# Optimization experiments

Measured on AMD Instinct MI355X. Metric: run time of the kernel, lower is better.

## Reference

```python
import jax, jax.numpy as jnp
import numpy as np

N = 4096
NFEAT = 1024
NHID = 512
NCLS = 32
NLAYERS = 3
SPARSITY = 0.002


def _l2norm(x, eps=1e-12):
    n = jnp.sqrt(jnp.sum(x * x, axis=1, keepdims=True))
    return x / jnp.maximum(n, eps)


def setup_inputs() -> dict:
    key = jax.random.key(0)
    ks = jax.random.split(key, 12)
    # sparse-valued dense adjacency (original stores torch.sparse but densifies every hop)
    vals = jax.random.uniform(ks[0], (N, N), dtype=jnp.float32)
    mask = jax.random.uniform(ks[1], (N, N)) < SPARSITY
    adj = jnp.where(mask, vals, 0.0)
    features = jax.random.normal(ks[2], (N, NFEAT), dtype=jnp.float32)
    # y is a one-hot label matrix [N, nclass]
    labels = jax.random.randint(ks[3], (N,), 0, NCLS)
    y = jax.nn.one_hot(labels, NCLS, dtype=jnp.float32)
    s = 0.02
    W0 = jax.random.normal(ks[4], (NFEAT + 3 * NCLS, NHID), dtype=jnp.float32) * s
    b0 = jnp.zeros((NHID,), jnp.float32)
    W1_0 = jax.random.normal(ks[5], (NHID + 3 * NCLS, NHID), dtype=jnp.float32) * s
    b1_0 = jnp.zeros((NHID,), jnp.float32)
    W1_1 = jax.random.normal(ks[6], (NHID + 3 * NCLS, NHID), dtype=jnp.float32) * s
    b1_1 = jnp.zeros((NHID,), jnp.float32)
    W2 = jax.random.normal(ks[7], (NFEAT + NHID, NCLS), dtype=jnp.float32) * s
    b2 = jnp.zeros((NCLS,), jnp.float32)
    alphas = jnp.ones((NLAYERS, 5), jnp.float32)
    return {
        "adj": adj, "features": features, "y": y,
        "W0": W0, "b0": b0, "W1_0": W1_0, "b1_0": b1_0,
        "W1_1": W1_1, "b1_1": b1_1, "W2": W2, "b2": b2,
        "alphas": alphas, "layer_norm": 1,
    }


def reference(adj, features, y, W0, b0, W1_0, b1_0, W1_1, b1_1, W2, b2, alphas, layer_norm):
    Ws = [(W0, b0), (W1_0, b1_0), (W1_1, b1_1)]
    initial_features = jax.lax.stop_gradient(features)  # .clone().detach()
    feats = features
    max_features = None
    pow_adj = adj  # persists across layers (faithful to original): hops adj, adj^2, adj^4
    for i in range(NLAYERS):
        mask_alpha = jax.nn.softmax(alphas[i], axis=0)
        for _ in range(i):
            pow_adj = adj @ pow_adj
        hop = pow_adj @ feats                                   # [N, d]
        dist = (pow_adj > 0).astype(adj.dtype)                  # binarized reachability
        y_out = dist @ y                                        # [N, c]
        y_in = dist.T @ y                                       # [N, c]
        y_all = y_in + y_out
        hop = mask_alpha[0] * hop
        y_out = mask_alpha[1] * y_out
        y_in = mask_alpha[2] * y_in
        y_all = mask_alpha[3] * y_all
        mat = jnp.concatenate([hop, y_out, y_in, y_all], axis=1)
        W, b = Ws[i]
        tmp = mat @ W + b
        if layer_norm:
            tmp = _l2norm(tmp)
        feats = tmp
        max_features = tmp if max_features is None else jnp.maximum(max_features, tmp)
    final_mat = jnp.concatenate([initial_features, max_features], axis=1)
    out = jax.nn.relu(final_mat)
    # dropout: eval mode (identity)
    out = out @ W2 + b2
    return jax.nn.log_softmax(out, axis=1)
```

## Files before the change

kernel.cpp:

```cpp
#include <hip/hip_runtime.h>
#include <hip/hip_bf16.h>
#include <math.h>

typedef unsigned long long u64;
typedef unsigned short ushort_t;
typedef float f32x4 __attribute__((ext_vector_type(4)));
typedef short s16x8 __attribute__((ext_vector_type(8)));

#define NN 4096
#define NF 1024
#define NH 512
#define NC 32
#define LDP 40
#define K0 (NF + 3*NC)
#define K1 (NH + 3*NC)

__device__ inline float bf2f(ushort_t u) {
    unsigned int v = ((unsigned int)u) << 16;
    return __uint_as_float(v);
}
__device__ inline ushort_t f2bf(float f) {
    __hip_bfloat16 h = __float2bfloat16(f);
    return *(ushort_t*)&h;
}

__global__ __launch_bounds__(64) void k_build(const float* __restrict__ adj, u64* __restrict__ B1,
                                              int* __restrict__ rowcnt, int* __restrict__ colidx,
                                              float* __restrict__ vals) {
    int i = blockIdx.x;
    int l = threadIdx.x;
    const float* row = adj + (size_t)i * NN + l * 64;
    const float4* row4 = (const float4*)row;
    u64 w = 0;
    #pragma unroll
    for (int k = 0; k < 16; ++k) {
        float4 v = row4[k];
        if (v.x > 0.f) w |= 1ULL << (4*k + 0);
        if (v.y > 0.f) w |= 1ULL << (4*k + 1);
        if (v.z > 0.f) w |= 1ULL << (4*k + 2);
        if (v.w > 0.f) w |= 1ULL << (4*k + 3);
    }
    B1[(size_t)i*64 + l] = w;
    int cnt = __popcll(w);
    int pre = cnt;
    #pragma unroll
    for (int o = 1; o < 64; o <<= 1) {
        int u = __shfl_up(pre, o, 64);
        if (l >= o) pre += u;
    }
    int excl = pre - cnt;
    int total = __shfl(pre, 63, 64);
    u64 ww = w;
    int idx = excl;
    while (ww) {
        int b = __ffsll((unsigned long long)ww) - 1;
        ww &= ww - 1;
        if (idx < 64) {
            colidx[i*64 + idx] = l*64 + b;
            vals[i*64 + idx] = row[b];
        }
        ++idx;
    }
    int tot = total < 64 ? total : 64;
    for (int s = tot + l; s < 64; s += 64) {
        colidx[i*64 + s] = 0;
        vals[i*64 + s] = 0.f;
    }
    if (l == 0) {
        int r4 = (tot + 3) & ~3;
        rowcnt[i] = r4 < 64 ? r4 : 64;
    }
}

__global__ __launch_bounds__(256) void k_prep(const float* __restrict__ features,
                                              __hip_bfloat16* __restrict__ featb,
                                              const float* __restrict__ y, u64* __restrict__ LC,
                                              const float* __restrict__ W0,
                                              const float* __restrict__ W1_0,
                                              const float* __restrict__ W1_1,
                                              __hip_bfloat16* __restrict__ Wt0,
                                              __hip_bfloat16* __restrict__ Wt1,
                                              __hip_bfloat16* __restrict__ Wt2,
                                              const float* __restrict__ alphas,
                                              float* __restrict__ a_sm) {
    __shared__ float tile[32][33];
    int b = blockIdx.x;
    int t = threadIdx.x;
    if (b < 4096) {
        int base = b * 1024 + t * 4;
        float4 v = *(const float4*)&features[base];
        ushort4 o;
        o.x = f2bf(v.x); o.y = f2bf(v.y); o.z = f2bf(v.z); o.w = f2bf(v.w);
        *(ushort4*)&((ushort_t*)featb)[base] = o;
    } else if (b < 4112) {
        int w = (b - 4096) * 4 + (t >> 6);
        int l = t & 63;
        const float* yr = y + (size_t)(w*64 + l) * NC;
        for (int c = 0; c < NC; ++c) {
            u64 m = __ballot(yr[c] > 0.5f);
            if (l == c) LC[c*64 + w] = m;
        }
    } else {
        const float* W; __hip_bfloat16* Wt; int K, ktiles, idx;
        if (b < 4672)      { W = W0;   Wt = Wt0; K = K0; ktiles = 35; idx = b - 4112; }
        else if (b < 4976) { W = W1_0; Wt = Wt1; K = K1; ktiles = 19; idx = b - 4672; }
        else if (b < 5280) { W = W1_1; Wt = Wt2; K = K1; ktiles = 19; idx = b - 4976; }
        else {
            if (t == 0) {
                for (int i = 0; i < 3; ++i) {
                    float m = -1e30f;
                    for (int j = 0; j < 5; ++j) m = fmaxf(m, alphas[i*5+j]);
                    float e[5]; float s = 0.f;
                    for (int j = 0; j < 5; ++j) { e[j] = expf(alphas[i*5+j] - m); s += e[j]; }
                    for (int j = 0; j < 5; ++j) a_sm[i*5+j] = e[j] / s;
                }
            }
            return;
        }
        int kb = (idx % ktiles) * 32, nb = (idx / ktiles) * 32;
        int tc = t & 31, tr8 = t >> 5;
        for (int r = tr8; r < 32; r += 8)
            tile[r][tc] = W[(size_t)(kb + r) * NH + nb + tc];
        __syncthreads();
        ushort_t* Wu = (ushort_t*)Wt;
        for (int r = tr8; r < 32; r += 8)
            Wu[(size_t)(nb + r) * K + kb + tc] = f2bf(tile[tc][r]);
    }
}

__global__ __launch_bounds__(256) void k_bsquare(const u64* __restrict__ Bidx,
                                                 const u64* __restrict__ Bdat,
                                                 u64* __restrict__ Bout) {
    int i = blockIdx.x;
    int t = threadIdx.x;
    int wid = t >> 6, lane = t & 63;
    __shared__ u64 ridx[64];
    __shared__ u64 part[4][64];
    if (t < 64) ridx[t] = Bidx[(size_t)i*64 + t];
    __syncthreads();
    u64 acc = 0;
    for (int u = wid*16; u < wid*16 + 16; ++u) {
        u64 w = ridx[u];
        while (w) {
            int k = u*64 + (__ffsll((unsigned long long)w) - 1);
            w &= (w - 1);
            acc |= Bdat[(size_t)k*64 + lane];
        }
    }
    part[wid][lane] = acc;
    __syncthreads();
    if (t < 64) Bout[(size_t)i*64 + t] = part[0][t] | part[1][t] | part[2][t] | part[3][t];
}

__global__ void k_btrans(const u64* __restrict__ B1, const u64* __restrict__ B2,
                         const u64* __restrict__ B4, u64* __restrict__ B1T,
                         u64* __restrict__ B2T, u64* __restrict__ B4T) {
    const u64* B; u64* BT;
    switch (blockIdx.z) {
        case 0: B = B1; BT = B1T; break;
        case 1: B = B2; BT = B2T; break;
        default: B = B4; BT = B4T; break;
    }
    int I = blockIdx.x, J = blockIdx.y;
    int t = threadIdx.x;
    __shared__ u64 ld[64];
    ld[t] = B[(size_t)(I*64 + t)*64 + J];
    __syncthreads();
    u64 out = 0;
    for (int r = 0; r < 64; ++r) out |= ((ld[r] >> t) & 1ULL) << r;
    BT[(size_t)(J*64 + t)*64 + I] = out;
}

__global__ __launch_bounds__(256) void k_ymat(const u64* __restrict__ B1, const u64* __restrict__ B1T,
                       const u64* __restrict__ B2, const u64* __restrict__ B2T,
                       const u64* __restrict__ B4, const u64* __restrict__ B4T,
                       const u64* __restrict__ LC, const float* __restrict__ a_sm,
                       __hip_bfloat16* __restrict__ mat0, __hip_bfloat16* __restrict__ mat1,
                       __hip_bfloat16* __restrict__ mat2) {
    int layer = blockIdx.y;
    const u64 *B, *BT; const float* asp; ushort_t* m; int d, K;
    if (layer == 0)      { B = B1; BT = B1T; asp = a_sm;      m = (ushort_t*)mat0; d = NF; K = K0; }
    else if (layer == 1) { B = B2; BT = B2T; asp = a_sm + 5;  m = (ushort_t*)mat1; d = NH; K = K1; }
    else                 { B = B4; BT = B4T; asp = a_sm + 10; m = (ushort_t*)mat2; d = NH; K = K1; }
    __shared__ u64 LCt[64 * 32];
    __shared__ u64 rows[8][64], rowsT[8][64];
    int rb = blockIdx.x * 8;
    int t = threadIdx.x;
    for (int k = t; k < 2048; k += 256) {
        int c = k >> 6, w = k & 63;
        LCt[w*32 + c] = LC[k];
    }
    for (int k = t; k < 512; k += 256) {
        int r = k >> 6, w = k & 63;
        rows[r][w]  = B[(size_t)(rb + r)*64 + w];
        rowsT[r][w] = BT[(size_t)(rb + r)*64 + w];
    }
    __syncthreads();
    int wid = t >> 6, lane = t & 63;
    int h = lane >> 5, c = lane & 31;
    int r = wid * 2 + h;
    int co = 0, ci = 0;
    #pragma unroll
    for (int w = 0; w < 64; ++w) {
        u64 lc = LCt[w*32 + c];
        co += __popcll(rows[r][w]  & lc);
        ci += __popcll(rowsT[r][w] & lc);
    }
    float a1 = asp[1], a2 = asp[2], a3 = asp[3];
    size_t i = rb + r;
    m[i*K + d + c]      = f2bf(a1 * (float)co);
    m[i*K + d + 32 + c] = f2bf(a2 * (float)ci);
    m[i*K + d + 64 + c] = f2bf(a3 * (float)(co + ci));
}

__global__ void k_spmm(const int* __restrict__ rowcnt, const int* __restrict__ colidx,
                       const float* __restrict__ vals, const __hip_bfloat16* __restrict__ X,
                       __hip_bfloat16* __restrict__ Y, int d, int ystride,
                       const float* __restrict__ a_sm, int ai) {
    int i = blockIdx.x * 4 + threadIdx.y;
    int t = threadIdx.x;
    int cnt = rowcnt[i];
    const ushort_t* Xu = (const ushort_t*)X;
    float acc[8] = {0,0,0,0,0,0,0,0};
    for (int p = 0; p < cnt; p += 4) {
        int4   cc = *(const int4*)&colidx[i*64 + p];
        float4 vv = *(const float4*)&vals[i*64 + p];
        s16x8 x0 = *(const s16x8*)&Xu[(size_t)cc.x * d + 8*t];
        s16x8 x1 = *(const s16x8*)&Xu[(size_t)cc.y * d + 8*t];
        s16x8 x2 = *(const s16x8*)&Xu[(size_t)cc.z * d + 8*t];
        s16x8 x3 = *(const s16x8*)&Xu[(size_t)cc.w * d + 8*t];
        #pragma unroll
        for (int j = 0; j < 8; ++j) {
            acc[j] += vv.x * bf2f((ushort_t)x0[j]);
            acc[j] += vv.y * bf2f((ushort_t)x1[j]);
            acc[j] += vv.z * bf2f((ushort_t)x2[j]);
            acc[j] += vv.w * bf2f((ushort_t)x3[j]);
        }
    }
    float alpha = (ai >= 0) ? a_sm[ai] : 1.0f;
    s16x8 o;
    #pragma unroll
    for (int j = 0; j < 8; ++j) o[j] = (short)f2bf(alpha * acc[j]);
    *(s16x8*)&((ushort_t*)Y)[(size_t)i*ystride + 8*t] = o;
}

__global__ __launch_bounds__(256) void k_gemm_mfma(const __hip_bfloat16* __restrict__ mat,
                                                   const __hip_bfloat16* __restrict__ Wt,
                                                   const float* __restrict__ b,
                                                   float* __restrict__ C, int K) {
    __shared__ ushort_t As[64 * LDP];
    __shared__ ushort_t Bs[64 * LDP];
    int bx = blockIdx.x;
    int xcd = bx & 7, rest = bx >> 3;
    int nt = rest & 7, mt = (rest >> 3) * 8 + xcd;
    int bm = mt * 64, bn = nt * 64;
    int tid = threadIdx.x;
    int srow = tid >> 2, scol = (tid & 3) * 8;
    int wid = tid >> 6, lane = tid & 63;
    int fr = lane & 15, fk = (lane >> 4) * 8;
    f32x4 acc[4] = {{0,0,0,0},{0,0,0,0},{0,0,0,0},{0,0,0,0}};
    const ushort_t* Au = (const ushort_t*)mat + (size_t)(bm + srow) * K + scol;
    const ushort_t* Bu = (const ushort_t*)Wt  + (size_t)(bn + srow) * K + scol;
    for (int k0 = 0; k0 < K; k0 += 32) {
        *(s16x8*)&As[srow * LDP + scol] = *(const s16x8*)(Au + k0);
        *(s16x8*)&Bs[srow * LDP + scol] = *(const s16x8*)(Bu + k0);
        __syncthreads();
        s16x8 af = *(const s16x8*)&As[(wid * 16 + fr) * LDP + fk];
        #pragma unroll
        for (int j = 0; j < 4; ++j) {
            s16x8 bfv = *(const s16x8*)&Bs[(j * 16 + fr) * LDP + fk];
            acc[j] = __builtin_amdgcn_mfma_f32_16x16x32_bf16(af, bfv, acc[j], 0, 0, 0);
        }
        __syncthreads();
    }
    int drow = bm + wid * 16 + (lane >> 4) * 4;
    #pragma unroll
    for (int j = 0; j < 4; ++j) {
        int col = bn + j * 16 + fr;
        float bias = b[col];
        #pragma unroll
        for (int r = 0; r < 4; ++r)
            C[(size_t)(drow + r) * NH + col] = acc[j][r] + bias;
    }
}

__global__ void k_l2norm(const float* __restrict__ tmp, __hip_bfloat16* __restrict__ featsb,
                         float* __restrict__ maxf, const int* __restrict__ lnflag,
                         int first) {
    int i = blockIdx.x;
    int t = threadIdx.x;
    float v0 = tmp[(size_t)i*NH + t];
    float v1 = tmp[(size_t)i*NH + 256 + t];
    float ss = v0*v0 + v1*v1;
    __shared__ float red[4];
    #pragma unroll
    for (int o = 32; o > 0; o >>= 1) ss += __shfl_down(ss, o, 64);
    if ((t & 63) == 0) red[t >> 6] = ss;
    __syncthreads();
    float tot = red[0] + red[1] + red[2] + red[3];
    float scale = 1.0f;
    if (*lnflag) {
        float n = sqrtf(tot);
        scale = 1.0f / fmaxf(n, 1e-12f);
    }
    v0 *= scale; v1 *= scale;
    ushort_t* fb = (ushort_t*)featsb;
    fb[(size_t)i*NH + t]       = f2bf(v0);
    fb[(size_t)i*NH + 256 + t] = f2bf(v1);
    if (first) {
        maxf[(size_t)i*NH + t] = v0;
        maxf[(size_t)i*NH + 256 + t] = v1;
    } else {
        maxf[(size_t)i*NH + t] = fmaxf(maxf[(size_t)i*NH + t], v0);
        maxf[(size_t)i*NH + 256 + t] = fmaxf(maxf[(size_t)i*NH + 256 + t], v1);
    }
}

__global__ __launch_bounds__(256) void k_l2final(const float* __restrict__ tmpo,
                                                 const float* __restrict__ maxf,
                                                 const float* __restrict__ feat0,
                                                 const float* __restrict__ W2,
                                                 const float* __restrict__ b2,
                                                 const int* __restrict__ lnflag,
                                                 float* __restrict__ out) {
    int rb = blockIdx.x * 8;
    int t = threadIdx.x;
    __shared__ float rows[8][NF + NH];
    __shared__ float part[8][8][32];
    for (int r = 0; r < 8; ++r) {
        const float* f0 = feat0 + (size_t)(rb + r) * NF;
        for (int c = t; c < NF; c += 256) rows[r][c] = fmaxf(f0[c], 0.f);
    }
    int wid = t >> 6, lane = t & 63;
    int ln = *lnflag;
    #pragma unroll
    for (int rr = 0; rr < 2; ++rr) {
        int r = wid * 2 + rr;
        const float4* tp = (const float4*)(tmpo + (size_t)(rb + r) * NH + lane * 8);
        float4 va = tp[0], vb = tp[1];
        float ss = va.x*va.x + va.y*va.y + va.z*va.z + va.w*va.w
                 + vb.x*vb.x + vb.y*vb.y + vb.z*vb.z + vb.w*vb.w;
        #pragma unroll
        for (int o = 32; o > 0; o >>= 1) ss += __shfl_xor(ss, o, 64);
        float scale = ln ? 1.0f / fmaxf(sqrtf(ss), 1e-12f) : 1.0f;
        const float4* mf = (const float4*)(maxf + (size_t)(rb + r) * NH + lane * 8);
        float4 ma = mf[0], mb = mf[1];
        float* dst = &rows[r][NF + lane * 8];
        dst[0] = fmaxf(fmaxf(ma.x, va.x*scale), 0.f);
        dst[1] = fmaxf(fmaxf(ma.y, va.y*scale), 0.f);
        dst[2] = fmaxf(fmaxf(ma.z, va.z*scale), 0.f);
        dst[3] = fmaxf(fmaxf(ma.w, va.w*scale), 0.f);
        dst[4] = fmaxf(fmaxf(mb.x, vb.x*scale), 0.f);
        dst[5] = fmaxf(fmaxf(mb.y, vb.y*scale), 0.f);
        dst[6] = fmaxf(fmaxf(mb.z, vb.z*scale), 0.f);
        dst[7] = fmaxf(fmaxf(mb.w, vb.w*scale), 0.f);
    }
    __syncthreads();
    int c = t & 31, g = t >> 5;
    float acc[8] = {0,0,0,0,0,0,0,0};
    for (int k = g * 192; k < (g + 1) * 192; ++k) {
        float w = W2[(size_t)k * NC + c];
        #pragma unroll
        for (int r = 0; r < 8; ++r) acc[r] += rows[r][k] * w;
    }
    #pragma unroll
    for (int r = 0; r < 8; ++r) part[g][r][c] = acc[r];
    __syncthreads();
    int r = g;
    float lg = b2[c];
    #pragma unroll
    for (int gg = 0; gg < 8; ++gg) lg += part[gg][r][c];
    float m = lg;
    #pragma unroll
    for (int o = 16; o > 0; o >>= 1) m = fmaxf(m, __shfl_xor(m, o, 32));
    float e = expf(lg - m), s = e;
    #pragma unroll
    for (int o = 16; o > 0; o >>= 1) s += __shfl_xor(s, o, 32);
    out[(size_t)(rb + r) * NC + c] = lg - m - logf(s);
}

extern "C" void kernel_launch(void* const* d_in, const int* in_sizes, int n_in,
                              void* d_out, int out_size, void* d_ws, size_t ws_size,
                              hipStream_t stream) {
    const float* adj      = (const float*)d_in[0];
    const float* features = (const float*)d_in[1];
    const float* y        = (const float*)d_in[2];
    const float* W0       = (const float*)d_in[3];
    const float* b0       = (const float*)d_in[4];
    const float* W1_0     = (const float*)d_in[5];
    const float* b1_0     = (const float*)d_in[6];
    const float* W1_1     = (const float*)d_in[7];
    const float* b1_1     = (const float*)d_in[8];
    const float* W2       = (const float*)d_in[9];
    const float* b2       = (const float*)d_in[10];
    const float* alphas   = (const float*)d_in[11];
    const int*   lnflag   = (const int*)d_in[12];
    float* out = (float*)d_out;

    char* ws = (char*)d_ws;
    size_t off = 0;
    auto alloc = [&](size_t bytes) -> char* {
        char* p = ws + off;
        off = (off + bytes + 255) & ~(size_t)255;
        return p;
    };
    float* a_sm   = (float*)alloc(16 * 4);
    int*   rowcnt = (int*)alloc((size_t)NN * 4);
    int*   colidx = (int*)alloc((size_t)NN * 64 * 4);
    float* vals   = (float*)alloc((size_t)NN * 64 * 4);
    u64* B1  = (u64*)alloc((size_t)NN * 64 * 8);
    u64* B2  = (u64*)alloc((size_t)NN * 64 * 8);
    u64* B4  = (u64*)alloc((size_t)NN * 64 * 8);
    u64* B1T = (u64*)alloc((size_t)NN * 64 * 8);
    u64* B2T = (u64*)alloc((size_t)NN * 64 * 8);
    u64* B4T = (u64*)alloc((size_t)NN * 64 * 8);
    u64* LC  = (u64*)alloc((size_t)NC * 64 * 8);
    __hip_bfloat16* featb  = (__hip_bfloat16*)alloc((size_t)NN * NF * 2);
    __hip_bfloat16* featsb = (__hip_bfloat16*)alloc((size_t)NN * NH * 2);
    __hip_bfloat16* t1b    = (__hip_bfloat16*)alloc((size_t)NN * NH * 2);
    __hip_bfloat16* mat0   = (__hip_bfloat16*)alloc((size_t)NN * K0 * 2);
    __hip_bfloat16* mat1   = (__hip_bfloat16*)alloc((size_t)NN * K1 * 2);
    __hip_bfloat16* mat2   = (__hip_bfloat16*)alloc((size_t)NN * K1 * 2);
    __hip_bfloat16* Wt0    = (__hip_bfloat16*)alloc((size_t)NH * K0 * 2);
    __hip_bfloat16* Wt1    = (__hip_bfloat16*)alloc((size_t)NH * K1 * 2);
    __hip_bfloat16* Wt2    = (__hip_bfloat16*)alloc((size_t)NH * K1 * 2);
    float* tmpo = (float*)alloc((size_t)NN * NH * 4);
    float* maxf = (float*)alloc((size_t)NN * NH * 4);
    __hip_bfloat16* t2b = (__hip_bfloat16*)tmpo;

    k_build<<<NN, 64, 0, stream>>>(adj, B1, rowcnt, colidx, vals);
    k_prep<<<5281, 256, 0, stream>>>(features, featb, y, LC, W0, W1_0, W1_1,
                                     Wt0, Wt1, Wt2, alphas, a_sm);
    k_bsquare<<<NN, 256, 0, stream>>>(B1, B1, B2);
    k_bsquare<<<NN, 256, 0, stream>>>(B2, B2, B4);
    k_btrans<<<dim3(64, 64, 3), 64, 0, stream>>>(B1, B2, B4, B1T, B2T, B4T);
    k_ymat<<<dim3(NN/8, 3), 256, 0, stream>>>(B1, B1T, B2, B2T, B4, B4T, LC, a_sm,
                                              mat0, mat1, mat2);

    k_spmm<<<NN/4, dim3(NF/8, 4), 0, stream>>>(rowcnt, colidx, vals, featb, mat0, NF, K0, a_sm, 0);
    k_gemm_mfma<<<512, 256, 0, stream>>>(mat0, Wt0, b0, tmpo, K0);
    k_l2norm<<<NN, 256, 0, stream>>>(tmpo, featsb, maxf, lnflag, 1);

    k_spmm<<<NN/4, dim3(NH/8, 4), 0, stream>>>(rowcnt, colidx, vals, featsb, t1b, NH, NH, a_sm, -1);
    k_spmm<<<NN/4, dim3(NH/8, 4), 0, stream>>>(rowcnt, colidx, vals, t1b, mat1, NH, K1, a_sm, 5);
    k_gemm_mfma<<<512, 256, 0, stream>>>(mat1, Wt1, b1_0, tmpo, K1);
    k_l2norm<<<NN, 256, 0, stream>>>(tmpo, featsb, maxf, lnflag, 0);

    k_spmm<<<NN/4, dim3(NH/8, 4), 0, stream>>>(rowcnt, colidx, vals, featsb, t1b, NH, NH, a_sm, -1);
    k_spmm<<<NN/4, dim3(NH/8, 4), 0, stream>>>(rowcnt, colidx, vals, t1b, t2b, NH, NH, a_sm, -1);
    k_spmm<<<NN/4, dim3(NH/8, 4), 0, stream>>>(rowcnt, colidx, vals, t2b, t1b, NH, NH, a_sm, -1);
    k_spmm<<<NN/4, dim3(NH/8, 4), 0, stream>>>(rowcnt, colidx, vals, t1b, mat2, NH, K1, a_sm, 10);
    k_gemm_mfma<<<512, 256, 0, stream>>>(mat2, Wt2, b1_1, tmpo, K1);

    k_l2final<<<NN/8, 256, 0, stream>>>(tmpo, maxf, features, W2, b2, lnflag, out);
}
```

Baseline: 223.3 us.

## Fuse pipeline into multi-role phase kernels with precomputed A² sparse matrix

```diff
diff --git a/kernel.cpp b/kernel.cpp
--- a/kernel.cpp
+++ b/kernel.cpp
@@ -24,11 +24,10 @@
     return *(ushort_t*)&h;
 }
 
-__global__ __launch_bounds__(64) void k_build(const float* __restrict__ adj, u64* __restrict__ B1,
-                                              int* __restrict__ rowcnt, int* __restrict__ colidx,
-                                              float* __restrict__ vals) {
-    int i = blockIdx.x;
-    int l = threadIdx.x;
+__device__ void role_build(int i, int l, const float* __restrict__ adj,
+                           u64* __restrict__ B1, int* __restrict__ rowcnt,
+                           int* __restrict__ rowcnt_true,
+                           int* __restrict__ colidx, float* __restrict__ vals) {
     const float* row = adj + (size_t)i * NN + l * 64;
     const float4* row4 = (const float4*)row;
     u64 w = 0;
@@ -67,56 +66,46 @@
         vals[i*64 + s] = 0.f;
     }
     if (l == 0) {
-        int r4 = (tot + 3) & ~3;
-        rowcnt[i] = r4 < 64 ? r4 : 64;
-    }
-}
-
-__global__ __launch_bounds__(256) void k_prep(const float* __restrict__ features,
-                                              __hip_bfloat16* __restrict__ featb,
-                                              const float* __restrict__ y, u64* __restrict__ LC,
-                                              const float* __restrict__ W0,
-                                              const float* __restrict__ W1_0,
-                                              const float* __restrict__ W1_1,
-                                              __hip_bfloat16* __restrict__ Wt0,
-                                              __hip_bfloat16* __restrict__ Wt1,
-                                              __hip_bfloat16* __restrict__ Wt2,
-                                              const float* __restrict__ alphas,
-                                              float* __restrict__ a_sm) {
-    __shared__ float tile[32][33];
+        rowcnt_true[i] = tot;
+        rowcnt[i] = (tot + 3) & ~3;
+    }
+}
+
+__global__ __launch_bounds__(256) void k_setup(const float* __restrict__ adj,
+        const float* __restrict__ features, __hip_bfloat16* __restrict__ featb,
+        const float* __restrict__ y, u64* __restrict__ LC,
+        const float* __restrict__ W0, const float* __restrict__ W1_0,
+        const float* __restrict__ W1_1,
+        __hip_bfloat16* __restrict__ Wt0, __hip_bfloat16* __restrict__ Wt1,
+        __hip_bfloat16* __restrict__ Wt2,
+        const float* __restrict__ alphas, float* __restrict__ a_sm,
+        u64* __restrict__ B1, int* __restrict__ rowcnt, int* __restrict__ rowcnt_true,
+        int* __restrict__ colidx, float* __restrict__ vals) {
+    __shared__ __align__(16) char smem[4352];
     int b = blockIdx.x;
     int t = threadIdx.x;
-    if (b < 4096) {
-        int base = b * 1024 + t * 4;
+    int wid = t >> 6, l = t & 63;
+    if (b < 1024) {
+        role_build(b*4 + wid, l, adj, B1, rowcnt, rowcnt_true, colidx, vals);
+    } else if (b < 5120) {
+        int base = (b - 1024) * 1024 + t * 4;
         float4 v = *(const float4*)&features[base];
         ushort4 o;
         o.x = f2bf(v.x); o.y = f2bf(v.y); o.z = f2bf(v.z); o.w = f2bf(v.w);
         *(ushort4*)&((ushort_t*)featb)[base] = o;
-    } else if (b < 4112) {
-        int w = (b - 4096) * 4 + (t >> 6);
-        int l = t & 63;
+    } else if (b < 5136) {
+        int w = (b - 5120) * 4 + wid;
         const float* yr = y + (size_t)(w*64 + l) * NC;
         for (int c = 0; c < NC; ++c) {
             u64 m = __ballot(yr[c] > 0.5f);
             if (l == c) LC[c*64 + w] = m;
         }
-    } else {
+    } else if (b < 6304) {
         const float* W; __hip_bfloat16* Wt; int K, ktiles, idx;
-        if (b < 4672)      { W = W0;   Wt = Wt0; K = K0; ktiles = 35; idx = b - 4112; }
-        else if (b < 4976) { W = W1_0; Wt = Wt1; K = K1; ktiles = 19; idx = b - 4672; }
-        else if (b < 5280) { W = W1_1; Wt = Wt2; K = K1; ktiles = 19; idx = b - 4976; }
-        else {
-            if (t == 0) {
-                for (int i = 0; i < 3; ++i) {
-                    float m = -1e30f;
-                    for (int j = 0; j < 5; ++j) m = fmaxf(m, alphas[i*5+j]);
-                    float e[5]; float s = 0.f;
-                    for (int j = 0; j < 5; ++j) { e[j] = expf(alphas[i*5+j] - m); s += e[j]; }
-                    for (int j = 0; j < 5; ++j) a_sm[i*5+j] = e[j] / s;
-                }
-            }
-            return;
-        }
+        if (b < 5696)      { W = W0;   Wt = Wt0; K = K0; ktiles = 35; idx = b - 5136; }
+        else if (b < 6000) { W = W1_0; Wt = Wt1; K = K1; ktiles = 19; idx = b - 5696; }
+        else               { W = W1_1; Wt = Wt2; K = K1; ktiles = 19; idx = b - 6000; }
+        float (*tile)[33] = (float(*)[33])smem;
         int kb = (idx % ktiles) * 32, nb = (idx / ktiles) * 32;
         int tc = t & 31, tr8 = t >> 5;
         for (int r = tr8; r < 32; r += 8)
@@ -125,17 +114,24 @@
         ushort_t* Wu = (ushort_t*)Wt;
         for (int r = tr8; r < 32; r += 8)
             Wu[(size_t)(nb + r) * K + kb + tc] = f2bf(tile[tc][r]);
-    }
-}
-
-__global__ __launch_bounds__(256) void k_bsquare(const u64* __restrict__ Bidx,
-                                                 const u64* __restrict__ Bdat,
-                                                 u64* __restrict__ Bout) {
-    int i = blockIdx.x;
-    int t = threadIdx.x;
+    } else {
+        if (t == 0) {
+            for (int i = 0; i < 3; ++i) {
+                float m = -1e30f;
+                for (int j = 0; j < 5; ++j) m = fmaxf(m, alphas[i*5+j]);
+                float e[5]; float s = 0.f;
+                for (int j = 0; j < 5; ++j) { e[j] = expf(alphas[i*5+j] - m); s += e[j]; }
+                for (int j = 0; j < 5; ++j) a_sm[i*5+j] = e[j] / s;
+            }
+        }
+    }
+}
+
+__device__ void role_bsq(int i, int t, char* smem, const u64* __restrict__ Bidx,
+                         const u64* __restrict__ Bdat, u64* __restrict__ Bout) {
+    u64* ridx = (u64*)smem;
+    u64* part = ridx + 64;
     int wid = t >> 6, lane = t & 63;
-    __shared__ u64 ridx[64];
-    __shared__ u64 part[4][64];
     if (t < 64) ridx[t] = Bidx[(size_t)i*64 + t];
     __syncthreads();
     u64 acc = 0;
@@ -147,53 +143,38 @@
             acc |= Bdat[(size_t)k*64 + lane];
         }
     }
-    part[wid][lane] = acc;
-    __syncthreads();
-    if (t < 64) Bout[(size_t)i*64 + t] = part[0][t] | part[1][t] | part[2][t] | part[3][t];
-}
-
-__global__ void k_btrans(const u64* __restrict__ B1, const u64* __restrict__ B2,
-                         const u64* __restrict__ B4, u64* __restrict__ B1T,
-                         u64* __restrict__ B2T, u64* __restrict__ B4T) {
-    const u64* B; u64* BT;
-    switch (blockIdx.z) {
-        case 0: B = B1; BT = B1T; break;
-        case 1: B = B2; BT = B2T; break;
-        default: B = B4; BT = B4T; break;
-    }
-    int I = blockIdx.x, J = blockIdx.y;
-    int t = threadIdx.x;
-    __shared__ u64 ld[64];
-    ld[t] = B[(size_t)(I*64 + t)*64 + J];
+    part[wid*64 + lane] = acc;
+    __syncthreads();
+    if (t < 64) Bout[(size_t)i*64 + t] = part[t] | part[64+t] | part[128+t] | part[192+t];
+}
+
+__device__ void role_btrans(int tb, int wid, int l, char* smem,
+                            const u64* __restrict__ B, u64* __restrict__ BT) {
+    u64* ld = ((u64*)smem) + wid*64;
+    int I = tb >> 6, J = tb & 63;
+    ld[l] = B[(size_t)(I*64 + l)*64 + J];
     __syncthreads();
     u64 out = 0;
-    for (int r = 0; r < 64; ++r) out |= ((ld[r] >> t) & 1ULL) << r;
-    BT[(size_t)(J*64 + t)*64 + I] = out;
-}
-
-__global__ __launch_bounds__(256) void k_ymat(const u64* __restrict__ B1, const u64* __restrict__ B1T,
-                       const u64* __restrict__ B2, const u64* __restrict__ B2T,
-                       const u64* __restrict__ B4, const u64* __restrict__ B4T,
-                       const u64* __restrict__ LC, const float* __restrict__ a_sm,
-                       __hip_bfloat16* __restrict__ mat0, __hip_bfloat16* __restrict__ mat1,
-                       __hip_bfloat16* __restrict__ mat2) {
-    int layer = blockIdx.y;
-    const u64 *B, *BT; const float* asp; ushort_t* m; int d, K;
-    if (layer == 0)      { B = B1; BT = B1T; asp = a_sm;      m = (ushort_t*)mat0; d = NF; K = K0; }
-    else if (layer == 1) { B = B2; BT = B2T; asp = a_sm + 5;  m = (ushort_t*)mat1; d = NH; K = K1; }
-    else                 { B = B4; BT = B4T; asp = a_sm + 10; m = (ushort_t*)mat2; d = NH; K = K1; }
-    __shared__ u64 LCt[64 * 32];
-    __shared__ u64 rows[8][64], rowsT[8][64];
-    int rb = blockIdx.x * 8;
-    int t = threadIdx.x;
+    #pragma unroll
+    for (int r = 0; r < 64; ++r) out |= ((ld[r] >> l) & 1ULL) << r;
+    BT[(size_t)(J*64 + l)*64 + I] = out;
+}
+
+__device__ void role_ymat(int rb, int t, char* smem, const u64* __restrict__ B,
+                          const u64* __restrict__ BT, const u64* __restrict__ LC,
+                          const float* __restrict__ asp, ushort_t* __restrict__ m,
+                          int d, int K) {
+    u64* LCt   = (u64*)smem;
+    u64* rows  = LCt + 64*32;
+    u64* rowsT = rows + 8*64;
     for (int k = t; k < 2048; k += 256) {
         int c = k >> 6, w = k & 63;
         LCt[w*32 + c] = LC[k];
     }
     for (int k = t; k < 512; k += 256) {
         int r = k >> 6, w = k & 63;
-        rows[r][w]  = B[(size_t)(rb + r)*64 + w];
-        rowsT[r][w] = BT[(size_t)(rb + r)*64 + w];
+        rows[r*64 + w]  = B[(size_t)(rb + r)*64 + w];
+        rowsT[r*64 + w] = BT[(size_t)(rb + r)*64 + w];
     }
     __syncthreads();
     int wid = t >> 6, lane = t & 63;
@@ -203,8 +184,8 @@
     #pragma unroll
     for (int w = 0; w < 64; ++w) {
         u64 lc = LCt[w*32 + c];
-        co += __popcll(rows[r][w]  & lc);
-        ci += __popcll(rowsT[r][w] & lc);
+        co += __popcll(rows[r*64 + w]  & lc);
+        ci += __popcll(rowsT[r*64 + w] & lc);
     }
     float a1 = asp[1], a2 = asp[2], a3 = asp[3];
     size_t i = rb + r;
@@ -213,22 +194,75 @@
     m[i*K + d + 64 + c] = f2bf(a3 * (float)(co + ci));
 }
 
-__global__ void k_spmm(const int* __restrict__ rowcnt, const int* __restrict__ colidx,
-                       const float* __restrict__ vals, const __hip_bfloat16* __restrict__ X,
-                       __hip_bfloat16* __restrict__ Y, int d, int ystride,
-                       const float* __restrict__ a_sm, int ai) {
-    int i = blockIdx.x * 4 + threadIdx.y;
-    int t = threadIdx.x;
-    int cnt = rowcnt[i];
-    const ushort_t* Xu = (const ushort_t*)X;
+__device__ void role_a2build(int i, int t, char* smem,
+                             const int* __restrict__ rowcnt_true,
+                             const int* __restrict__ colidx, const float* __restrict__ vals,
+                             int* __restrict__ colidx2, float* __restrict__ vals2,
+                             int* __restrict__ rowcnt2) {
+    float* colacc = (float*)smem;
+    int* wcnt = (int*)(smem + 16384);
+    for (int k = t; k < 4096; k += 256) colacc[k] = 0.f;
+    __syncthreads();
+    int wid = t >> 6, l = t & 63;
+    int cti = rowcnt_true[i];
+    for (int p = 0; p < cti; ++p) {
+        int j = colidx[i*64 + p];
+        float vij = vals[i*64 + p];
+        int ctj = rowcnt_true[j];
+        if (l < ctj) {
+            int k = colidx[j*64 + l];
+            float vjk = vals[j*64 + l];
+            if ((k >> 10) == wid) colacc[k] += vij * vjk;
+        }
+    }
+    __syncthreads();
+    int cnt_w = 0;
+    for (int c = 0; c < 16; ++c) {
+        float v = colacc[wid*1024 + c*64 + l];
+        u64 mm = __ballot(v != 0.f);
+        cnt_w += __popcll(mm);
+    }
+    if (l == 0) wcnt[wid] = cnt_w;
+    __syncthreads();
+    int prefix = 0;
+    for (int wq = 0; wq < wid; ++wq) prefix += wcnt[wq];
+    int total = wcnt[0] + wcnt[1] + wcnt[2] + wcnt[3];
+    int pos = prefix;
+    for (int c = 0; c < 16; ++c) {
+        int col = wid*1024 + c*64 + l;
+        float v = colacc[col];
+        u64 mm = __ballot(v != 0.f);
+        if (v != 0.f) {
+            int off2 = __popcll(mm & ((1ULL << l) - 1ULL));
+            int s = pos + off2;
+            if (s < 128) { colidx2[(size_t)i*128 + s] = col; vals2[(size_t)i*128 + s] = v; }
+        }
+        pos += __popcll(mm);
+    }
+    int tot2 = total < 128 ? total : 128;
+    for (int s = tot2 + t; s < 128; s += 256) {
+        colidx2[(size_t)i*128 + s] = 0;
+        vals2[(size_t)i*128 + s] = 0.f;
+    }
+    if (t == 0) {
+        int r4 = (tot2 + 3) & ~3;
+        rowcnt2[i] = r4 < 128 ? r4 : 128;
+    }
+}
+
+__device__ void role_spmm_bf(int i, int tx, const int* __restrict__ rc,
+                             const int* __restrict__ ci, const float* __restrict__ vl,
+                             int cap, const ushort_t* __restrict__ X, int d,
+                             ushort_t* __restrict__ Y, int ystride, float alpha) {
+    int cnt = rc[i];
     float acc[8] = {0,0,0,0,0,0,0,0};
     for (int p = 0; p < cnt; p += 4) {
-        int4   cc = *(const int4*)&colidx[i*64 + p];
-        float4 vv = *(const float4*)&vals[i*64 + p];
-        s16x8 x0 = *(const s16x8*)&Xu[(size_t)cc.x * d + 8*t];
-        s16x8 x1 = *(const s16x8*)&Xu[(size_t)cc.y * d + 8*t];
-        s16x8 x2 = *(const s16x8*)&Xu[(size_t)cc.z * d + 8*t];
-        s16x8 x3 = *(const s16x8*)&Xu[(size_t)cc.w * d + 8*t];
+        int4   cc = *(const int4*)&ci[(size_t)i*cap + p];
+        float4 vv = *(const float4*)&vl[(size_t)i*cap + p];
+        s16x8 x0 = *(const s16x8*)&X[(size_t)cc.x * d + 8*tx];
+        s16x8 x1 = *(const s16x8*)&X[(size_t)cc.y * d + 8*tx];
+        s16x8 x2 = *(const s16x8*)&X[(size_t)cc.z * d + 8*tx];
+        s16x8 x3 = *(const s16x8*)&X[(size_t)cc.w * d + 8*tx];
         #pragma unroll
         for (int j = 0; j < 8; ++j) {
             acc[j] += vv.x * bf2f((ushort_t)x0[j]);
@@ -237,30 +271,58 @@
             acc[j] += vv.w * bf2f((ushort_t)x3[j]);
         }
     }
-    float alpha = (ai >= 0) ? a_sm[ai] : 1.0f;
     s16x8 o;
     #pragma unroll
     for (int j = 0; j < 8; ++j) o[j] = (short)f2bf(alpha * acc[j]);
-    *(s16x8*)&((ushort_t*)Y)[(size_t)i*ystride + 8*t] = o;
-}
-
-__global__ __launch_bounds__(256) void k_gemm_mfma(const __hip_bfloat16* __restrict__ mat,
-                                                   const __hip_bfloat16* __restrict__ Wt,
-                                                   const float* __restrict__ b,
-                                                   float* __restrict__ C, int K) {
-    __shared__ ushort_t As[64 * LDP];
-    __shared__ ushort_t Bs[64 * LDP];
-    int bx = blockIdx.x;
+    *(s16x8*)&Y[(size_t)i*ystride + 8*tx] = o;
+}
+
+__device__ void role_spmm_f32s(int i, int tx, const int* __restrict__ rc,
+                               const int* __restrict__ ci, const float* __restrict__ vl,
+                               const float* __restrict__ src, const float* __restrict__ parts,
+                               int ln, ushort_t* __restrict__ Y, int ystride, float alpha) {
+    int cnt = rc[i];
+    float acc[8] = {0,0,0,0,0,0,0,0};
+    for (int p = 0; p < cnt; p += 4) {
+        int4   cc = *(const int4*)&ci[(size_t)i*128 + p];
+        float4 vv = *(const float4*)&vl[(size_t)i*128 + p];
+        int cols[4] = {cc.x, cc.y, cc.z, cc.w};
+        float vs4[4] = {vv.x, vv.y, vv.z, vv.w};
+        #pragma unroll
+        for (int e = 0; e < 4; ++e) {
+            int col = cols[e];
+            float4 pa = *(const float4*)&parts[col*8];
+            float4 pb = *(const float4*)&parts[col*8 + 4];
+            float ss = pa.x+pa.y+pa.z+pa.w + pb.x+pb.y+pb.z+pb.w;
+            float sc = ln ? 1.0f / fmaxf(sqrtf(ss), 1e-12f) : 1.0f;
+            float vsc = vs4[e] * sc;
+            float4 xa = *(const float4*)&src[(size_t)col*NH + 8*tx];
+            float4 xb = *(const float4*)&src[(size_t)col*NH + 8*tx + 4];
+            acc[0] += vsc*xa.x; acc[1] += vsc*xa.y; acc[2] += vsc*xa.z; acc[3] += vsc*xa.w;
+            acc[4] += vsc*xb.x; acc[5] += vsc*xb.y; acc[6] += vsc*xb.z; acc[7] += vsc*xb.w;
+        }
+    }
+    s16x8 o;
+    #pragma unroll
+    for (int j = 0; j < 8; ++j) o[j] = (short)f2bf(alpha * acc[j]);
+    *(s16x8*)&Y[(size_t)i*ystride + 8*tx] = o;
+}
+
+__device__ void role_gemm(int bx, int tid, char* smem,
+                          const ushort_t* __restrict__ mat, const ushort_t* __restrict__ Wt,
+                          const float* __restrict__ bias, float* __restrict__ C,
+                          float* __restrict__ parts, int K) {
+    ushort_t* As = (ushort_t*)smem;
+    ushort_t* Bs = As + 64*LDP;
     int xcd = bx & 7, rest = bx >> 3;
     int nt = rest & 7, mt = (rest >> 3) * 8 + xcd;
     int bm = mt * 64, bn = nt * 64;
-    int tid = threadIdx.x;
     int srow = tid >> 2, scol = (tid & 3) * 8;
     int wid = tid >> 6, lane = tid & 63;
-    int fr = lane & 15, fk = (lane >> 4) * 8;
+    int fr = lane & 15, hi2 = lane >> 4, fk = hi2 * 8;
     f32x4 acc[4] = {{0,0,0,0},{0,0,0,0},{0,0,0,0},{0,0,0,0}};
-    const ushort_t* Au = (const ushort_t*)mat + (size_t)(bm + srow) * K + scol;
-    const ushort_t* Bu = (const ushort_t*)Wt  + (size_t)(bn + srow) * K + scol;
+    const ushort_t* Au = mat + (size_t)(bm + srow) * K + scol;
+    const ushort_t* Bu = Wt  + (size_t)(bn + srow) * K + scol;
     for (int k0 = 0; k0 < K; k0 += 32) {
         *(s16x8*)&As[srow * LDP + scol] = *(const s16x8*)(Au + k0);
         *(s16x8*)&Bs[srow * LDP + scol] = *(const s16x8*)(Bu + k0);
@@ -273,56 +335,148 @@
         }
         __syncthreads();
     }
-    int drow = bm + wid * 16 + (lane >> 4) * 4;
+    int drow = bm + wid * 16 + hi2 * 4;
+    #pragma unroll
+    for (int r = 0; r < 4; ++r) {
+        float ps = 0.f;
+        #pragma unroll
+        for (int j = 0; j < 4; ++j) ps += acc[j][r] * acc[j][r];
+        ps = 0.f;
+        #pragma unroll
+        for (int j = 0; j < 4; ++j) {
+            float v = acc[j][r] + bias[bn + j*16 + fr];
+            ps += v * v;
+        }
+        #pragma unroll
+        for (int o = 1; o < 16; o <<= 1) ps += __shfl_xor(ps, o, 64);
+        if (fr == 0) parts[(size_t)(drow + r) * 8 + nt] = ps;
+    }
     #pragma unroll
     for (int j = 0; j < 4; ++j) {
         int col = bn + j * 16 + fr;
-        float bias = b[col];
+        float bv = bias[col];
         #pragma unroll
         for (int r = 0; r < 4; ++r)
-            C[(size_t)(drow + r) * NH + col] = acc[j][r] + bias;
-    }
-}
-
-__global__ void k_l2norm(const float* __restrict__ tmp, __hip_bfloat16* __restrict__ featsb,
-                         float* __restrict__ maxf, const int* __restrict__ lnflag,
-                         int first) {
-    int i = blockIdx.x;
+            C[(size_t)(drow + r) * NH + col] = acc[j][r] + bv;
+    }
+}
+
+__global__ __launch_bounds__(256) void k_phase2(const u64* __restrict__ B1, u64* __restrict__ B2,
+        u64* __restrict__ B1T,
+        const int* __restrict__ rowcnt_true, const int* __restrict__ colidx,
+        const float* __restrict__ vals,
+        int* __restrict__ colidx2, float* __restrict__ vals2, int* __restrict__ rowcnt2,
+        const int* __restrict__ rowcnt, const __hip_bfloat16* __restrict__ featb,
+        __hip_bfloat16* __restrict__ mat0, const float* __restrict__ a_sm) {
+    __shared__ __align__(16) char smem[16512];
+    int b = blockIdx.x;
     int t = threadIdx.x;
-    float v0 = tmp[(size_t)i*NH + t];
-    float v1 = tmp[(size_t)i*NH + 256 + t];
-    float ss = v0*v0 + v1*v1;
-    __shared__ float red[4];
-    #pragma unroll
-    for (int o = 32; o > 0; o >>= 1) ss += __shfl_down(ss, o, 64);
-    if ((t & 63) == 0) red[t >> 6] = ss;
-    __syncthreads();
-    float tot = red[0] + red[1] + red[2] + red[3];
-    float scale = 1.0f;
-    if (*lnflag) {
-        float n = sqrtf(tot);
-        scale = 1.0f / fmaxf(n, 1e-12f);
-    }
-    v0 *= scale; v1 *= scale;
-    ushort_t* fb = (ushort_t*)featsb;
-    fb[(size_t)i*NH + t]       = f2bf(v0);
-    fb[(size_t)i*NH + 256 + t] = f2bf(v1);
-    if (first) {
-        maxf[(size_t)i*NH + t] = v0;
-        maxf[(size_t)i*NH + 256 + t] = v1;
+    int wid = t >> 6, l = t & 63;
+    if (b < 4096) {
+        role_bsq(b, t, smem, B1, B1, B2);
+    } else if (b < 5120) {
+        role_btrans((b - 4096)*4 + wid, wid, l, smem, B1, B1T);
+    } else if (b < 9216) {
+        role_a2build(b - 5120, t, smem, rowcnt_true, colidx, vals, colidx2, vals2, rowcnt2);
     } else {
-        maxf[(size_t)i*NH + t] = fmaxf(maxf[(size_t)i*NH + t], v0);
-        maxf[(size_t)i*NH + 256 + t] = fmaxf(maxf[(size_t)i*NH + 256 + t], v1);
-    }
-}
-
-__global__ __launch_bounds__(256) void k_l2final(const float* __restrict__ tmpo,
-                                                 const float* __restrict__ maxf,
-                                                 const float* __restrict__ feat0,
-                                                 const float* __restrict__ W2,
-                                                 const float* __restrict__ b2,
-                                                 const int* __restrict__ lnflag,
-                                                 float* __restrict__ out) {
+        int idx = b - 9216;
+        int ty = t >> 7, tx = t & 127;
+        role_spmm_bf(idx*2 + ty, tx, rowcnt, colidx, vals, 64,
+                     (const ushort_t*)featb, NF, (ushort_t*)mat0, K0, a_sm[0]);
+    }
+}
+
+__global__ __launch_bounds__(256) void k_phase3(const u64* __restrict__ B2, u64* __restrict__ B4,
+        u64* __restrict__ B2T, const u64* __restrict__ B1, const u64* __restrict__ B1T,
+        const u64* __restrict__ LC, const float* __restrict__ a_sm,
+        __hip_bfloat16* __restrict__ mat0) {
+    __shared__ __align__(16) char smem[24576];
+    int b = blockIdx.x;
+    int t = threadIdx.x;
+    int wid = t >> 6, l = t & 63;
+    if (b < 4096) {
+        role_bsq(b, t, smem, B2, B2, B4);
+    } else if (b < 5120) {
+        role_btrans((b - 4096)*4 + wid, wid, l, smem, B2, B2T);
+    } else {
+        role_ymat((b - 5120)*8, t, smem, B1, B1T, LC, a_sm, (ushort_t*)mat0, NF, K0);
+    }
+}
+
+__global__ __launch_bounds__(256) void k_phase4(const __hip_bfloat16* __restrict__ mat0,
+        const __hip_bfloat16* __restrict__ Wt0, const float* __restrict__ b0,
+        float* __restrict__ tmp0, float* __restrict__ parts0,
+        const u64* __restrict__ B4, u64* __restrict__ B4T,
+        const u64* __restrict__ B2, const u64* __restrict__ B2T,
+        const u64* __restrict__ LC, const float* __restrict__ a_sm,
+        __hip_bfloat16* __restrict__ mat1) {
+    __shared__ __align__(16) char smem[24576];
+    int b = blockIdx.x;
+    int t = threadIdx.x;
+    int wid = t >> 6, l = t & 63;
+    if (b < 512) {
+        role_gemm(b, t, smem, (const ushort_t*)mat0, (const ushort_t*)Wt0, b0,
+                  tmp0, parts0, K0);
+    } else if (b < 1536) {
+        role_btrans((b - 512)*4 + wid, wid, l, smem, B4, B4T);
+    } else {
+        role_ymat((b - 1536)*8, t, smem, B2, B2T, LC, a_sm + 5, (ushort_t*)mat1, NH, K1);
+    }
+}
+
+__global__ __launch_bounds__(256) void k_phase5(const int* __restrict__ rowcnt2,
+        const int* __restrict__ colidx2, const float* __restrict__ vals2,
+        const float* __restrict__ tmp0, const float* __restrict__ parts0,
+        const int* __restrict__ lnflag, __hip_bfloat16* __restrict__ mat1,
+        const u64* __restrict__ B4, const u64* __restrict__ B4T,
+        const u64* __restrict__ LC, const float* __restrict__ a_sm,
+        __hip_bfloat16* __restrict__ mat2) {
+    __shared__ __align__(16) char smem[24576];
+    int b = blockIdx.x;
+    int t = threadIdx.x;
+    if (b < 1024) {
+        int i = b*4 + (t >> 6), tx = t & 63;
+        role_spmm_f32s(i, tx, rowcnt2, colidx2, vals2, tmp0, parts0, *lnflag,
+                       (ushort_t*)mat1, K1, a_sm[5]);
+    } else {
+        role_ymat((b - 1024)*8, t, smem, B4, B4T, LC, a_sm + 10, (ushort_t*)mat2, NH, K1);
+    }
+}
+
+__global__ __launch_bounds__(256) void k_gemm(const __hip_bfloat16* __restrict__ mat,
+        const __hip_bfloat16* __restrict__ Wt, const float* __restrict__ bias,
+        float* __restrict__ C, float* __restrict__ parts, int K) {
+    __shared__ __align__(16) char smem[2 * 64 * LDP * 2];
+    role_gemm(blockIdx.x, threadIdx.x, smem, (const ushort_t*)mat, (const ushort_t*)Wt,
+              bias, C, parts, K);
+}
+
+__global__ __launch_bounds__(256) void k_spmm_f(const int* __restrict__ rc2,
+        const int* __restrict__ ci2, const float* __restrict__ vl2,
+        const float* __restrict__ src, const float* __restrict__ parts,
+        const int* __restrict__ lnflag, __hip_bfloat16* __restrict__ Y,
+        int ystride, const float* __restrict__ a_sm, int ai) {
+    int i = blockIdx.x*4 + (threadIdx.x >> 6), tx = threadIdx.x & 63;
+    float alpha = (ai >= 0) ? a_sm[ai] : 1.0f;
+    role_spmm_f32s(i, tx, rc2, ci2, vl2, src, parts, *lnflag, (ushort_t*)Y, ystride, alpha);
+}
+
+__global__ __launch_bounds__(256) void k_spmm_b(const int* __restrict__ rc2,
+        const int* __restrict__ ci2, const float* __restrict__ vl2,
+        const __hip_bfloat16* __restrict__ X, __hip_bfloat16* __restrict__ Y,
+        int ystride, const float* __restrict__ a_sm, int ai) {
+    int i = blockIdx.x*4 + (threadIdx.x >> 6), tx = threadIdx.x & 63;
+    float alpha = (ai >= 0) ? a_sm[ai] : 1.0f;
+    role_spmm_bf(i, tx, rc2, ci2, vl2, 128, (const ushort_t*)X, NH, (ushort_t*)Y,
+                 ystride, alpha);
+}
+
+__global__ __launch_bounds__(256) void k_l2final(const float* __restrict__ tmp0,
+        const float* __restrict__ parts0, const float* __restrict__ tmp1,
+        const float* __restrict__ parts1, const float* __restrict__ tmp2,
+        const float* __restrict__ parts2, const float* __restrict__ feat0,
+        const float* __restrict__ W2, const float* __restrict__ b2,
+        const int* __restrict__ lnflag, float* __restrict__ out) {
     int rb = blockIdx.x * 8;
     int t = threadIdx.x;
     __shared__ float rows[8][NF + NH];
@@ -336,24 +490,31 @@
     #pragma unroll
     for (int rr = 0; rr < 2; ++rr) {
         int r = wid * 2 + rr;
-        const float4* tp = (const float4*)(tmpo + (size_t)(rb + r) * NH + lane * 8);
-        float4 va = tp[0], vb = tp[1];
-        float ss = va.x*va.x + va.y*va.y + va.z*va.z + va.w*va.w
-                 + vb.x*vb.x + vb.y*vb.y + vb.z*vb.z + vb.w*vb.w;
-        #pragma unroll
-        for (int o = 32; o > 0; o >>= 1) ss += __shfl_xor(ss, o, 64);
-        float scale = ln ? 1.0f / fmaxf(sqrtf(ss), 1e-12f) : 1.0f;
-        const float4* mf = (const float4*)(maxf + (size_t)(rb + r) * NH + lane * 8);
-        float4 ma = mf[0], mb = mf[1];
+        int row = rb + r;
+        float s0, s1, s2;
+        {
+            float4 a0 = *(const float4*)&parts0[row*8], b0v = *(const float4*)&parts0[row*8+4];
+            float4 a1 = *(const float4*)&parts1[row*8], b1v = *(const float4*)&parts1[row*8+4];
+            float4 a2 = *(const float4*)&parts2[row*8], b2v = *(const float4*)&parts2[row*8+4];
+            float q0 = a0.x+a0.y+a0.z+a0.w + b0v.x+b0v.y+b0v.z+b0v.w;
+            float q1 = a1.x+a1.y+a1.z+a1.w + b1v.x+b1v.y+b1v.z+b1v.w;
+            float q2 = a2.x+a2.y+a2.z+a2.w + b2v.x+b2v.y+b2v.z+b2v.w;
+            s0 = ln ? 1.0f / fmaxf(sqrtf(q0), 1e-12f) : 1.0f;
+            s1 = ln ? 1.0f / fmaxf(sqrtf(q1), 1e-12f) : 1.0f;
+            s2 = ln ? 1.0f / fmaxf(sqrtf(q2), 1e-12f) : 1.0f;
+        }
+        const float4* t0 = (const float4*)(tmp0 + (size_t)row * NH + lane * 8);
+        const float4* t1 = (const float4*)(tmp1 + (size_t)row * NH + lane * 8);
+        const float4* t2 = (const float4*)(tmp2 + (size_t)row * NH + lane * 8);
         float* dst = &rows[r][NF + lane * 8];
-        dst[0] = fmaxf(fmaxf(ma.x, va.x*scale), 0.f);
-        dst[1] = fmaxf(fmaxf(ma.y, va.y*scale), 0.f);
-        dst[2] = fmaxf(fmaxf(ma.z, va.z*scale), 0.f);
-        dst[3] = fmaxf(fmaxf(ma.w, va.w*scale), 0.f);
-        dst[4] = fmaxf(fmaxf(mb.x, vb.x*scale), 0.f);
-        dst[5] = fmaxf(fmaxf(mb.y, vb.y*scale), 0.f);
-        dst[6] = fmaxf(fmaxf(mb.z, vb.z*scale), 0.f);
-        dst[7] = fmaxf(fmaxf(mb.w, vb.w*scale), 0.f);
+        #pragma unroll
+        for (int h = 0; h < 2; ++h) {
+            float4 v0 = t0[h], v1 = t1[h], v2 = t2[h];
+            dst[h*4+0] = fmaxf(fmaxf(fmaxf(v0.x*s0, v1.x*s1), v2.x*s2), 0.f);
+            dst[h*4+1] = fmaxf(fmaxf(fmaxf(v0.y*s0, v1.y*s1), v2.y*s2), 0.f);
+            dst[h*4+2] = fmaxf(fmaxf(fmaxf(v0.z*s0, v1.z*s1), v2.z*s2), 0.f);
+            dst[h*4+3] = fmaxf(fmaxf(fmaxf(v0.w*s0, v1.w*s1), v2.w*s2), 0.f);
+        }
     }
     __syncthreads();
     int c = t & 31, g = t >> 5;
@@ -404,10 +565,14 @@
         off = (off + bytes + 255) & ~(size_t)255;
         return p;
     };
-    float* a_sm   = (float*)alloc(16 * 4);
-    int*   rowcnt = (int*)alloc((size_t)NN * 4);
-    int*   colidx = (int*)alloc((size_t)NN * 64 * 4);
-    float* vals   = (float*)alloc((size_t)NN * 64 * 4);
+    float* a_sm        = (float*)alloc(16 * 4);
+    int*   rowcnt      = (int*)alloc((size_t)NN * 4);
+    int*   rowcnt_true = (int*)alloc((size_t)NN * 4);
+    int*   colidx      = (int*)alloc((size_t)NN * 64 * 4);
+    float* vals        = (float*)alloc((size_t)NN * 64 * 4);
+    int*   colidx2     = (int*)alloc((size_t)NN * 128 * 4);
+    float* vals2       = (float*)alloc((size_t)NN * 128 * 4);
+    int*   rowcnt2     = (int*)alloc((size_t)NN * 4);
     u64* B1  = (u64*)alloc((size_t)NN * 64 * 8);
     u64* B2  = (u64*)alloc((size_t)NN * 64 * 8);
     u64* B4  = (u64*)alloc((size_t)NN * 64 * 8);
@@ -415,42 +580,36 @@
     u64* B2T = (u64*)alloc((size_t)NN * 64 * 8);
     u64* B4T = (u64*)alloc((size_t)NN * 64 * 8);
     u64* LC  = (u64*)alloc((size_t)NC * 64 * 8);
-    __hip_bfloat16* featb  = (__hip_bfloat16*)alloc((size_t)NN * NF * 2);
-    __hip_bfloat16* featsb = (__hip_bfloat16*)alloc((size_t)NN * NH * 2);
-    __hip_bfloat16* t1b    = (__hip_bfloat16*)alloc((size_t)NN * NH * 2);
-    __hip_bfloat16* mat0   = (__hip_bfloat16*)alloc((size_t)NN * K0 * 2);
-    __hip_bfloat16* mat1   = (__hip_bfloat16*)alloc((size_t)NN * K1 * 2);
-    __hip_bfloat16* mat2   = (__hip_bfloat16*)alloc((size_t)NN * K1 * 2);
-    __hip_bfloat16* Wt0    = (__hip_bfloat16*)alloc((size_t)NH * K0 * 2);
-    __hip_bfloat16* Wt1    = (__hip_bfloat16*)alloc((size_t)NH * K1 * 2);
-    __hip_bfloat16* Wt2    = (__hip_bfloat16*)alloc((size_t)NH * K1 * 2);
-    float* tmpo = (float*)alloc((size_t)NN * NH * 4);
-    float* maxf = (float*)alloc((size_t)NN * NH * 4);
-    __hip_bfloat16* t2b = (__hip_bfloat16*)tmpo;
-
-    k_build<<<NN, 64, 0, stream>>>(adj, B1, rowcnt, colidx, vals);
-    k_prep<<<5281, 256, 0, stream>>>(features, featb, y, LC, W0, W1_0, W1_1,
-                                     Wt0, Wt1, Wt2, alphas, a_sm);
-    k_bsquare<<<NN, 256, 0, stream>>>(B1, B1, B2);
-    k_bsquare<<<NN, 256, 0, stream>>>(B2, B2, B4);
-    k_btrans<<<dim3(64, 64, 3), 64, 0, stream>>>(B1, B2, B4, B1T, B2T, B4T);
-    k_ymat<<<dim3(NN/8, 3), 256, 0, stream>>>(B1, B1T, B2, B2T, B4, B4T, LC, a_sm,
-                                              mat0, mat1, mat2);
-
-    k_spmm<<<NN/4, dim3(NF/8, 4), 0, stream>>>(rowcnt, colidx, vals, featb, mat0, NF, K0, a_sm, 0);
-    k_gemm_mfma<<<512, 256, 0, stream>>>(mat0, Wt0, b0, tmpo, K0);
-    k_l2norm<<<NN, 256, 0, stream>>>(tmpo, featsb, maxf, lnflag, 1);
-
-    k_spmm<<<NN/4, dim3(NH/8, 4), 0, stream>>>(rowcnt, colidx, vals, featsb, t1b, NH, NH, a_sm, -1);
-    k_spmm<<<NN/4, dim3(NH/8, 4), 0, stream>>>(rowcnt, colidx, vals, t1b, mat1, NH, K1, a_sm, 5);
-    k_gemm_mfma<<<512, 256, 0, stream>>>(mat1, Wt1, b1_0, tmpo, K1);
-    k_l2norm<<<NN, 256, 0, stream>>>(tmpo, featsb, maxf, lnflag, 0);
-
-    k_spmm<<<NN/4, dim3(NH/8, 4), 0, stream>>>(rowcnt, colidx, vals, featsb, t1b, NH, NH, a_sm, -1);
-    k_spmm<<<NN/4, dim3(NH/8, 4), 0, stream>>>(rowcnt, colidx, vals, t1b, t2b, NH, NH, a_sm, -1);
-    k_spmm<<<NN/4, dim3(NH/8, 4), 0, stream>>>(rowcnt, colidx, vals, t2b, t1b, NH, NH, a_sm, -1);
-    k_spmm<<<NN/4, dim3(NH/8, 4), 0, stream>>>(rowcnt, colidx, vals, t1b, mat2, NH, K1, a_sm, 10);
-    k_gemm_mfma<<<512, 256, 0, stream>>>(mat2, Wt2, b1_1, tmpo, K1);
-
-    k_l2final<<<NN/8, 256, 0, stream>>>(tmpo, maxf, features, W2, b2, lnflag, out);
-}
+    __hip_bfloat16* featb = (__hip_bfloat16*)alloc((size_t)NN * NF * 2);
+    __hip_bfloat16* t1b   = (__hip_bfloat16*)alloc((size_t)NN * NH * 2);
+    __hip_bfloat16* mat0  = (__hip_bfloat16*)alloc((size_t)NN * K0 * 2);
+    __hip_bfloat16* mat1  = (__hip_bfloat16*)alloc((size_t)NN * K1 * 2);
+    __hip_bfloat16* mat2  = (__hip_bfloat16*)alloc((size_t)NN * K1 * 2);
+    __hip_bfloat16* Wt0   = (__hip_bfloat16*)alloc((size_t)NH * K0 * 2);
+    __hip_bfloat16* Wt1   = (__hip_bfloat16*)alloc((size_t)NH * K1 * 2);
+    __hip_bfloat16* Wt2   = (__hip_bfloat16*)alloc((size_t)NH * K1 * 2);
+    float* tmp0   = (float*)alloc((size_t)NN * NH * 4);
+    float* tmp1   = (float*)alloc((size_t)NN * NH * 4);
+    float* tmp2   = (float*)alloc((size_t)NN * NH * 4);
+    float* parts0 = (float*)alloc((size_t)NN * 8 * 4);
+    float* parts1 = (float*)alloc((size_t)NN * 8 * 4);
+    float* parts2 = (float*)alloc((size_t)NN * 8 * 4);
+
+    k_setup<<<6305, 256, 0, stream>>>(adj, features, featb, y, LC, W0, W1_0, W1_1,
+                                      Wt0, Wt1, Wt2, alphas, a_sm,
+                                      B1, rowcnt, rowcnt_true, colidx, vals);
+    k_phase2<<<11264, 256, 0, stream>>>(B1, B2, B1T, rowcnt_true, colidx, vals,
+                                        colidx2, vals2, rowcnt2, rowcnt, featb, mat0, a_sm);
+    k_phase3<<<5632, 256, 0, stream>>>(B2, B4, B2T, B1, B1T, LC, a_sm, mat0);
+    k_phase4<<<2048, 256, 0, stream>>>(mat0, Wt0, b0, tmp0, parts0,
+                                       B4, B4T, B2, B2T, LC, a_sm, mat1);
+    k_phase5<<<1536, 256, 0, stream>>>(rowcnt2, colidx2, vals2, tmp0, parts0, lnflag,
+                                       mat1, B4, B4T, LC, a_sm, mat2);
+    k_gemm<<<512, 256, 0, stream>>>(mat1, Wt1, b1_0, tmp1, parts1, K1);
+    k_spmm_f<<<NN/4, 256, 0, stream>>>(rowcnt2, colidx2, vals2, tmp1, parts1, lnflag,
+                                       t1b, NH, a_sm, -1);
+    k_spmm_b<<<NN/4, 256, 0, stream>>>(rowcnt2, colidx2, vals2, t1b, mat2, K1, a_sm, 10);
+    k_gemm<<<512, 256, 0, stream>>>(mat2, Wt2, b1_1, tmp2, parts2, K1);
+    k_l2final<<<NN/8, 256, 0, stream>>>(tmp0, parts0, tmp1, parts1, tmp2, parts2,
+                                        features, W2, b2, lnflag, out);
+}
```

Measured after the change: 319.3 us. 1.43x slower.
